# Kernel tuning notes

Measured on AMD Instinct MI355X. Metric: run time of the kernel, lower is better.

Reference implementation:

```python
import jax, jax.numpy as jnp
import numpy as np

PATCH_SIZE = [3, 5, 7]
PATCH_SEQ = [5, 7]
SEQ_SIZE = 6
WIN = 210
D_MODEL = 256
B, M = 8, 55
EPS = 1e-5


def _loo(p):
    # leave-one-out index matrix, row i = all indices except i -> (p, p-1)
    return np.array([[k for k in range(p) if k != i] for i in range(p)], dtype=np.int32)


def _mlp(x, W1, b1, W2, b2):
    # torch MLP: fc2(relu(fc1(x))), Linear weights are (out, in)
    h = jax.nn.relu(x @ W1.T + b1)
    return h @ W2.T + b2


def _forward(x, sP, nP, ssP, nsP):
    Bn, L, Mn = x.shape
    # RevIN 'norm' with fresh affine (weight=1, bias=0): identity affine; stats detached
    mean = jax.lax.stop_gradient(jnp.mean(x, axis=1, keepdims=True))
    std = jax.lax.stop_gradient(jnp.sqrt(jnp.var(x, axis=1, keepdims=True) + EPS))
    xn = (x - mean) / std
    xt = jnp.transpose(xn, (0, 2, 1)).reshape(Bn * Mn, L)  # (BM, L)
    sm, pm, ssr, psr = [], [], [], []
    for j, p in enumerate(PATCH_SIZE):
        n = L // p
        x3 = xt.reshape(Bn * Mn, p, n)  # l = r*n + k
        # size branch: leave-one-out over the p axis, blocks ordered i*n + k
        feat = jnp.transpose(x3[:, _loo(p), :], (0, 1, 3, 2)).reshape(Bn * Mn, L, p - 1)
        y = _mlp(feat, *sP[j])[..., 0]  # (BM, L)
        sm.append(jnp.transpose(y.reshape(Bn, Mn, L), (0, 2, 1)))
        # num branch: leave-one-out over the n axis of row l%p, leaving out column l//p
        g = _mlp(x3[:, :, _loo(n)], *nP[j])[..., 0]  # (BM, p, n)
        # torch cats over l (axis 0) then reshapes (B, M, L): flat order is (l, b, m)
        prior = jnp.transpose(g, (2, 1, 0)).reshape(Bn, Mn, L)  # faithful scrambled reshape
        pm.append(jnp.transpose(prior, (0, 2, 1)))
    s = SEQ_SIZE
    for j, p in enumerate(PATCH_SEQ):
        n = L // (p * s)
        x4 = xt.reshape(Bn * Mn, p, n, s)  # l = (r*n + k)*s + t
        # size_seq branch: leave-one-out over p, feature = (p-1)*s per (i, k) position
        feat = jnp.transpose(x4[:, _loo(p)], (0, 1, 3, 2, 4)).reshape(Bn * Mn, p * n, (p - 1) * s)
        y = _mlp(feat, *ssP[j])  # (BM, p*n, s)
        ssr.append(jnp.transpose(y.reshape(Bn, Mn, L), (0, 2, 1)))
        # num_seq branch: leave-one-out over n, cat order i*p + r
        featn = jnp.transpose(x4[:, :, _loo(n), :], (0, 2, 1, 3, 4)).reshape(Bn * Mn, n * p, (n - 1) * s)
        g = _mlp(featn, *nsP[j])  # (BM, n*p, s)
        d0 = PATCH_SEQ[0]  # original code hardcodes patch_seq[0] here
        h = jnp.transpose(g.reshape(Bn, Mn, (n * p) // d0, d0, s), (0, 1, 3, 2, 4)).reshape(Bn, Mn, L)
        psr.append(jnp.transpose(h, (0, 2, 1)))
    # original returns 4 lists of (B, L, M); stack all 10 for a single output
    return jnp.stack(sm + pm + ssr + psr, axis=0)


def setup_inputs() -> dict:
    key = jax.random.key(0)
    keys = iter(jax.random.split(key, 128))
    d = {"x": jax.random.normal(next(keys), (B, WIN, M), dtype=jnp.float32)}

    def lin(name, out_d, in_d):
        d[name + "W"] = jax.random.normal(next(keys), (out_d, in_d), dtype=jnp.float32) / np.float32(np.sqrt(in_d))
        d[name + "b"] = jax.random.normal(next(keys), (out_d,), dtype=jnp.float32) * np.float32(0.01)

    for j, p in enumerate(PATCH_SIZE):
        lin(f"s1_{j}", D_MODEL, p - 1)
        lin(f"s2_{j}", 1, D_MODEL)
        lin(f"n1_{j}", D_MODEL, WIN // p - 1)
        lin(f"n2_{j}", 1, D_MODEL)
    for j, p in enumerate(PATCH_SEQ):
        lin(f"ss1_{j}", D_MODEL, (p - 1) * SEQ_SIZE)
        lin(f"ss2_{j}", SEQ_SIZE, D_MODEL)
        lin(f"ns1_{j}", D_MODEL, WIN // p - SEQ_SIZE)
        lin(f"ns2_{j}", SEQ_SIZE, D_MODEL)
    return d


def reference(x, s1_0W, s1_0b, s2_0W, s2_0b, n1_0W, n1_0b, n2_0W, n2_0b,
              s1_1W, s1_1b, s2_1W, s2_1b, n1_1W, n1_1b, n2_1W, n2_1b,
              s1_2W, s1_2b, s2_2W, s2_2b, n1_2W, n1_2b, n2_2W, n2_2b,
              ss1_0W, ss1_0b, ss2_0W, ss2_0b, ns1_0W, ns1_0b, ns2_0W, ns2_0b,
              ss1_1W, ss1_1b, ss2_1W, ss2_1b, ns1_1W, ns1_1b, ns2_1W, ns2_1b):
    sP = [(s1_0W, s1_0b, s2_0W, s2_0b), (s1_1W, s1_1b, s2_1W, s2_1b), (s1_2W, s1_2b, s2_2W, s2_2b)]
    nP = [(n1_0W, n1_0b, n2_0W, n2_0b), (n1_1W, n1_1b, n2_1W, n2_1b), (n1_2W, n1_2b, n2_2W, n2_2b)]
    ssP = [(ss1_0W, ss1_0b, ss2_0W, ss2_0b), (ss1_1W, ss1_1b, ss2_1W, ss2_1b)]
    nsP = [(ns1_0W, ns1_0b, ns2_0W, ns2_0b), (ns1_1W, ns1_1b, ns2_1W, ns2_1b)]
    return _forward(x, sP, nP, ssP, nsP)
```

## Files before the change

kernel.cpp:

```cpp
#include <hip/hip_runtime.h>

#define LL  210
#define MM  55
#define NBM 440
#define DM  256
#define MLT 11550
#define BLM 92400

__device__ __forceinline__ float wave_sum(float v) {
#pragma unroll
    for (int off = 32; off > 0; off >>= 1) v += __shfl_xor(v, off, 64);
    return v;
}

__device__ __forceinline__ void fma4(float4& a, const float4 w, const float s) {
    a.x += w.x * s; a.y += w.y * s; a.z += w.z * s; a.w += w.w * s;
}
__device__ __forceinline__ void fms4(float4& a, const float4 w, const float s) {
    a.x -= w.x * s; a.y -= w.y * s; a.z -= w.z * s; a.w -= w.w * s;
}

__global__ __launch_bounds__(256) void knorm_trans(
        const float* __restrict__ x,
        const float* __restrict__ nw0, const float* __restrict__ nw1,
        const float* __restrict__ nw2,
        float* __restrict__ xt, float* __restrict__ w1t) {
    __shared__ float red[4];
    const int t = threadIdx.x;
    if (blockIdx.x < NBM) {
        const int bm = blockIdx.x, b = bm / MM, m = bm % MM;
        const int wid = t >> 6, lane = t & 63;
        float v = (t < LL) ? x[b * MLT + t * MM + m] : 0.f;
        float sv = wave_sum(v);
        if (lane == 0) red[wid] = sv;
        __syncthreads();
        float mean = (red[0] + red[1] + red[2] + red[3]) * (1.f / 210.f);
        __syncthreads();
        float dv = (t < LL) ? v - mean : 0.f;
        float sq = wave_sum(dv * dv);
        if (lane == 0) red[wid] = sq;
        __syncthreads();
        float var = (red[0] + red[1] + red[2] + red[3]) * (1.f / 210.f);
        float inv = rsqrtf(var + 1e-5f);
        if (t < LL) xt[bm * LL + t] = dv * inv;
    } else {
        int e = (int)(blockIdx.x - NBM) * 256 + t;
        const float* src; int ind, off, rel;
        if (e < 69 * DM)       { src = nw0; ind = 69; off = 0;        rel = e; }
        else if (e < 110 * DM) { src = nw1; ind = 41; off = 69 * DM;  rel = e - 69 * DM; }
        else                   { src = nw2; ind = 29; off = 110 * DM; rel = e - 110 * DM; }
        int d = rel / ind, k = rel - d * ind;
        w1t[off + k * DM + d] = src[d * ind + k];
    }
}

template <int IND>
__device__ __forceinline__ void ksize_body(const float* __restrict__ xt,
        const float* __restrict__ W1, const float* __restrict__ b1,
        const float* __restrict__ W2, const float* __restrict__ b2,
        int bm, int j, float* __restrict__ smem, float* __restrict__ out) {
    constexpr int P = IND + 1;
    constexpr int N = LL / P;
    constexpr int WPAD = (IND == 2) ? 2 : ((IND == 4) ? 4 : 8);
    float* w1p = smem;
    float* bw  = smem + DM * 8;
    float* xs  = smem + DM * 10;
    const int t = threadIdx.x;
    if (t < LL) xs[t] = xt[bm * LL + t];
    bw[2 * t]     = b1[t];
    bw[2 * t + 1] = W2[t];
    for (int e = t; e < DM * WPAD; e += 256) {
        int d = e / WPAD, c = e - d * WPAD;
        w1p[e] = (c < IND) ? W1[d * IND + c] : 0.f;
    }
    __syncthreads();
    if (t >= LL) return;
    const int l = t, i = l / N, k = l - i * N;
    float f[IND];
#pragma unroll
    for (int idx = 0; idx < IND; ++idx) {
        int row = idx < i ? idx : idx + 1;
        f[idx] = xs[row * N + k];
    }
    float y = b2[0];
#pragma unroll 4
    for (int d = 0; d < DM; ++d) {
        const float2 bwv = *(const float2*)&bw[2 * d];
        float acc = bwv.x;
        if constexpr (WPAD == 2) {
            const float2 w = *(const float2*)&w1p[d * 2];
            acc += w.x * f[0] + w.y * f[1];
        } else if constexpr (WPAD == 4) {
            const float4 w = *(const float4*)&w1p[d * 4];
            acc += w.x * f[0] + w.y * f[1] + w.z * f[2] + w.w * f[3];
        } else {
            const float4 wa = *(const float4*)&w1p[d * 8];
            const float4 wb = *(const float4*)&w1p[d * 8 + 4];
            acc += wa.x * f[0] + wa.y * f[1] + wa.z * f[2] + wa.w * f[3]
                 + wb.x * f[4] + wb.y * f[5];
        }
        y += fmaxf(acc, 0.f) * bwv.y;
    }
    const int b = bm / MM, m = bm - b * MM;
    out[j * BLM + b * MLT + l * MM + m] = y;
}

__global__ __launch_bounds__(256) void ksize_all(const float* __restrict__ xt,
        const float* __restrict__ W1_0, const float* __restrict__ b1_0, const float* __restrict__ W2_0, const float* __restrict__ b2_0,
        const float* __restrict__ W1_1, const float* __restrict__ b1_1, const float* __restrict__ W2_1, const float* __restrict__ b2_1,
        const float* __restrict__ W1_2, const float* __restrict__ b1_2, const float* __restrict__ W2_2, const float* __restrict__ b2_2,
        float* __restrict__ out) {
    __shared__ __align__(16) float smem[DM * 10 + LL];
    const int blk = blockIdx.x;
    if (blk < NBM)           ksize_body<2>(xt, W1_0, b1_0, W2_0, b2_0, blk,           0, smem, out);
    else if (blk < 2 * NBM)  ksize_body<4>(xt, W1_1, b1_1, W2_1, b2_1, blk - NBM,     1, smem, out);
    else                     ksize_body<6>(xt, W1_2, b1_2, W2_2, b2_2, blk - 2 * NBM, 2, smem, out);
}

template <int P, int N>
__device__ __forceinline__ void knum_body(const float* __restrict__ xt,
        const float* __restrict__ wt, const float* __restrict__ b1,
        const float* __restrict__ W2, const float* __restrict__ b2,
        int r, int bm0, int j, float* __restrict__ xl, float* __restrict__ out) {
    const int t = threadIdx.x;
    for (int e = t; e < 8 * N; e += 256) {
        int g = e / N, q = e - g * N;
        xl[q * 8 + g] = xt[(bm0 + g) * LL + r * N + q];
    }
    if (t < 8) xl[N * 8 + t] = 0.f;
    __syncthreads();
    const int wid = t >> 6, lane = t & 63;
    const int g0 = wid * 2;
    const float4 b1v = *(const float4*)&b1[lane * 4];
    const float4 w2v = *(const float4*)&W2[lane * 4];
    const float b2v = b2[0];
    float4 A0 = b1v, A1 = b1v;
    float4 B0 = make_float4(0.f, 0.f, 0.f, 0.f), B1 = B0;
#pragma unroll 4
    for (int q = 1; q < N; ++q) {
        const float4 w = *(const float4*)&wt[(q - 1) * DM + lane * 4];
        const float2 xv = *(const float2*)&xl[q * 8 + g0];
        fma4(B0, w, xv.x); fma4(B1, w, xv.y);
    }
    int adr[2][2];
#pragma unroll
    for (int s2 = 0; s2 < 2; ++s2) {
        int kk = lane + 64 * s2; int kc = kk < N ? kk : 0;
#pragma unroll
        for (int g = 0; g < 2; ++g) {
            int fi = (kc * P + r) * NBM + (bm0 + g0 + g);
            int ob = fi / MLT, rem = fi - ob * MLT;
            int om = rem / LL, ol = rem - om * LL;
            adr[s2][g] = (3 + j) * BLM + ob * MLT + ol * MM + om;
        }
    }
    float yA0 = 0.f, yA1 = 0.f, yB0 = 0.f, yB1 = 0.f;
#pragma unroll 2
    for (int k = 0; k < N; ++k) {
        const float4 w = *(const float4*)&wt[k * DM + lane * 4];
        const float2 xk  = *(const float2*)&xl[k * 8 + g0];
        const float2 xk1 = *(const float2*)&xl[(k + 1) * 8 + g0];
        float hx = fmaxf(A0.x + B0.x, 0.f), hy = fmaxf(A0.y + B0.y, 0.f);
        float hz = fmaxf(A0.z + B0.z, 0.f), hw = fmaxf(A0.w + B0.w, 0.f);
        float y0 = hx * w2v.x + hy * w2v.y + hz * w2v.z + hw * w2v.w;
        hx = fmaxf(A1.x + B1.x, 0.f); hy = fmaxf(A1.y + B1.y, 0.f);
        hz = fmaxf(A1.z + B1.z, 0.f); hw = fmaxf(A1.w + B1.w, 0.f);
        float y1 = hx * w2v.x + hy * w2v.y + hz * w2v.z + hw * w2v.w;
        y0 = wave_sum(y0); y1 = wave_sum(y1);
        if (k == lane)      { yA0 = y0; yA1 = y1; }
        if (k == lane + 64) { yB0 = y0; yB1 = y1; }
        fma4(A0, w, xk.x);  fma4(A1, w, xk.y);
        fms4(B0, w, xk1.x); fms4(B1, w, xk1.y);
    }
    if (lane < N)      { out[adr[0][0]] = yA0 + b2v; out[adr[0][1]] = yA1 + b2v; }
    if (lane + 64 < N) { out[adr[1][0]] = yB0 + b2v; out[adr[1][1]] = yB1 + b2v; }
}

__global__ __launch_bounds__(256) void knum_all(const float* __restrict__ xt,
        const float* __restrict__ w1t,
        const float* __restrict__ b1_0, const float* __restrict__ W2_0, const float* __restrict__ b2_0,
        const float* __restrict__ b1_1, const float* __restrict__ W2_1, const float* __restrict__ b2_1,
        const float* __restrict__ b1_2, const float* __restrict__ W2_2, const float* __restrict__ b2_2,
        float* __restrict__ out) {
    __shared__ __align__(16) float xl[71 * 8];
    const int blk = blockIdx.x;
    if (blk < 165) {
        int rel = blk;       int bm0 = (rel / 3) * 8, r = rel % 3;
        knum_body<3, 70>(xt, w1t,            b1_0, W2_0, b2_0, r, bm0, 0, xl, out);
    } else if (blk < 440) {
        int rel = blk - 165; int bm0 = (rel / 5) * 8, r = rel % 5;
        knum_body<5, 42>(xt, w1t + 69 * DM,  b1_1, W2_1, b2_1, r, bm0, 1, xl, out);
    } else {
        int rel = blk - 440; int bm0 = (rel / 7) * 8, r = rel % 7;
        knum_body<7, 30>(xt, w1t + 110 * DM, b1_2, W2_2, b2_2, r, bm0, 2, xl, out);
    }
}

template <int ISNUM, int P, int N>
__device__ __forceinline__ void kseq_body(const float* __restrict__ xt,
        const float* __restrict__ W1, const float* __restrict__ b1,
        const float* __restrict__ W2, const float* __restrict__ b2,
        int bm0, int slab, float* __restrict__ smem, float* __restrict__ out) {
    constexpr int NROWS = ISNUM ? (N - 1) : (P - 1);
    constexpr int IND = NROWS * 6;
    constexpr int WST = DM + 8;
    float* w1s  = smem;
    float* w2s  = smem + 36 * WST;
    float* b1s  = w2s + 6 * DM;
    float* b2s_ = b1s + DM;
    float* xl   = b2s_ + 8;
    const int t = threadIdx.x;
    for (int e = t; e < DM * IND; e += 256) {
        int d = e / IND, fi = e - d * IND;
        w1s[fi * WST + d] = W1[e];
    }
    for (int e = t; e < 6 * DM; e += 256) w2s[e] = W2[e];
    b1s[t] = b1[t];
    if (t < 6) b2s_[t] = b2[t];
    for (int e = t; e < 2 * LL; e += 256) {
        int g = e / LL, q = e - g * LL;
        xl[q * 2 + g] = xt[(bm0 + g) * LL + q];
    }
    __syncthreads();
    const int wid = t >> 6, lane = t & 63;
    const float4 b1v = *(const float4*)&b1s[lane * 4];
    for (int q = wid; q < 35; q += 4) {
        int a0, k0;
        if (ISNUM) { k0 = q / P; a0 = q - k0 * P; }
        else       { a0 = q / N; k0 = q - a0 * N; }
        const int pivot = ISNUM ? k0 : a0;
        float4 acc0 = b1v, acc1 = b1v;
#pragma unroll 2
        for (int idx = 0; idx < NROWS; ++idx) {
            int row = idx < pivot ? idx : idx + 1;
            int xbase = ISNUM ? (a0 * N + row) * 6 : (row * N + k0) * 6;
#pragma unroll
            for (int tt = 0; tt < 6; ++tt) {
                const float2 xv = *(const float2*)&xl[(xbase + tt) * 2];
                const float4 w = *(const float4*)&w1s[(idx * 6 + tt) * WST + lane * 4];
                fma4(acc0, w, xv.x); fma4(acc1, w, xv.y);
            }
        }
        acc0.x = fmaxf(acc0.x, 0.f); acc0.y = fmaxf(acc0.y, 0.f);
        acc0.z = fmaxf(acc0.z, 0.f); acc0.w = fmaxf(acc0.w, 0.f);
        acc1.x = fmaxf(acc1.x, 0.f); acc1.y = fmaxf(acc1.y, 0.f);
        acc1.z = fmaxf(acc1.z, 0.f); acc1.w = fmaxf(acc1.w, 0.f);
        float po0[6], po1[6];
#pragma unroll
        for (int tt = 0; tt < 6; ++tt) {
            const float4 w2v = *(const float4*)&w2s[tt * DM + lane * 4];
            float p0 = acc0.x * w2v.x + acc0.y * w2v.y + acc0.z * w2v.z + acc0.w * w2v.w;
            float p1 = acc1.x * w2v.x + acc1.y * w2v.y + acc1.z * w2v.z + acc1.w * w2v.w;
            po0[tt] = wave_sum(p0);
            po1[tt] = wave_sum(p1);
        }
        if (lane < 2) {
            const int bm = bm0 + lane;
            const int b = bm / MM, m = bm - b * MM;
            const int c2 = q / 5, dd = q - c2 * 5;
#pragma unroll
            for (int tt = 0; tt < 6; ++tt) {
                int l = ISNUM ? (dd * 42 + c2 * 6 + tt) : (q * 6 + tt);
                out[slab + b * MLT + l * MM + m] = (lane ? po1[tt] : po0[tt]) + b2s_[tt];
            }
        }
    }
}

__global__ __launch_bounds__(256) void kseq_all(const float* __restrict__ xt,
        const float* __restrict__ ss1W0, const float* __restrict__ ss1b0, const float* __restrict__ ss2W0, const float* __restrict__ ss2b0,
        const float* __restrict__ ss1W1, const float* __restrict__ ss1b1, const float* __restrict__ ss2W1, const float* __restrict__ ss2b1,
        const float* __restrict__ ns1W0, const float* __restrict__ ns1b0, const float* __restrict__ ns2W0, const float* __restrict__ ns2b0,
        const float* __restrict__ ns1W1, const float* __restrict__ ns1b1, const float* __restrict__ ns2W1, const float* __restrict__ ns2b1,
        float* __restrict__ out) {
    __shared__ __align__(16) float smem[36 * (DM + 8) + 6 * DM + DM + 8 + 2 * LL];
    const int blk = blockIdx.x;
    const int tc = blk / 220, bm0 = (blk - tc * 220) * 2;
    if (tc == 0)      kseq_body<0, 5, 7>(xt, ss1W0, ss1b0, ss2W0, ss2b0, bm0, 6 * BLM, smem, out);
    else if (tc == 1) kseq_body<0, 7, 5>(xt, ss1W1, ss1b1, ss2W1, ss2b1, bm0, 7 * BLM, smem, out);
    else if (tc == 2) kseq_body<1, 5, 7>(xt, ns1W0, ns1b0, ns2W0, ns2b0, bm0, 8 * BLM, smem, out);
    else              kseq_body<1, 7, 5>(xt, ns1W1, ns1b1, ns2W1, ns2b1, bm0, 9 * BLM, smem, out);
}

extern "C" void kernel_launch(void* const* d_in, const int* in_sizes, int n_in,
                              void* d_out, int out_size, void* d_ws, size_t ws_size,
                              hipStream_t stream) {
    (void)in_sizes; (void)n_in; (void)out_size; (void)ws_size;
    const float* x = (const float*)d_in[0];
    const float *s1W[3], *s1b[3], *s2W[3], *s2b[3], *n1W[3], *n1b[3], *n2W[3], *n2b[3];
    for (int j = 0; j < 3; ++j) {
        int base = 1 + j * 8;
        s1W[j] = (const float*)d_in[base + 0]; s1b[j] = (const float*)d_in[base + 1];
        s2W[j] = (const float*)d_in[base + 2]; s2b[j] = (const float*)d_in[base + 3];
        n1W[j] = (const float*)d_in[base + 4]; n1b[j] = (const float*)d_in[base + 5];
        n2W[j] = (const float*)d_in[base + 6]; n2b[j] = (const float*)d_in[base + 7];
    }
    const float *ss1W[2], *ss1b[2], *ss2W[2], *ss2b[2], *ns1W[2], *ns1b[2], *ns2W[2], *ns2b[2];
    for (int j = 0; j < 2; ++j) {
        int base = 25 + j * 8;
        ss1W[j] = (const float*)d_in[base + 0]; ss1b[j] = (const float*)d_in[base + 1];
        ss2W[j] = (const float*)d_in[base + 2]; ss2b[j] = (const float*)d_in[base + 3];
        ns1W[j] = (const float*)d_in[base + 4]; ns1b[j] = (const float*)d_in[base + 5];
        ns2W[j] = (const float*)d_in[base + 6]; ns2b[j] = (const float*)d_in[base + 7];
    }
    float* out = (float*)d_out;
    float* xt  = (float*)d_ws;
    float* w1t = xt + NBM * LL;

    knorm_trans<<<579, 256, 0, stream>>>(x, n1W[0], n1W[1], n1W[2], xt, w1t);
    ksize_all<<<1320, 256, 0, stream>>>(xt,
        s1W[0], s1b[0], s2W[0], s2b[0],
        s1W[1], s1b[1], s2W[1], s2b[1],
        s1W[2], s1b[2], s2W[2], s2b[2], out);
    knum_all<<<825, 256, 0, stream>>>(xt, w1t,
        n1b[0], n2W[0], n2b[0],
        n1b[1], n2W[1], n2b[1],
        n1b[2], n2W[2], n2b[2], out);
    kseq_all<<<880, 256, 0, stream>>>(xt,
        ss1W[0], ss1b[0], ss2W[0], ss2b[0],
        ss1W[1], ss1b[1], ss2W[1], ss2b[1],
        ns1W[0], ns1b[0], ns2W[0], ns2b[0],
        ns1W[1], ns1b[1], ns2W[1], ns2b[1], out);
}
```

Measured before the change: 260.6 us.

## Interleave normalized series in groups of eight and prepack all MLP weights globally

The normalization kernel now writes activations in an 8-series interleaved layout. It also pre-transposes the seq-branch first-layer weights and packs the size-branch weights into float4 records, so the consumer kernels read directly from global/L2 instead of staging through shared memory. The seq kernel processes 8 series per block with 8 accumulators, cutting the grid from 880 to 220 blocks. The num and seq kernels replace per-output wave reductions with a butterfly transpose-reduce that produces 8 results per pass. This removes shared-memory staging, syncs and redundant weight loads. In exchange it raises register pressure and gives fewer blocks in kseq, which may underfill the GPU.

```diff
diff --git a/kernel.cpp b/kernel.cpp
--- a/kernel.cpp
+++ b/kernel.cpp
@@ -7,6 +7,10 @@
 #define MLT 11550
 #define BLM 92400
 
+#define XTG_OFF  0
+#define W1T_OFF  92400
+#define REC_OFF  158704
+
 __device__ __forceinline__ float wave_sum(float v) {
 #pragma unroll
     for (int off = 32; off > 0; off >>= 1) v += __shfl_xor(v, off, 64);
@@ -20,15 +24,46 @@
     a.x -= w.x * s; a.y -= w.y * s; a.z -= w.z * s; a.w -= w.w * s;
 }
 
+__device__ __forceinline__ float bfly8(const float y[8], const int lane) {
+    float z[4];
+#pragma unroll
+    for (int i = 0; i < 4; ++i) {
+        float snd = (lane & 1) ? y[2*i] : y[2*i+1];
+        float rcv = __shfl_xor(snd, 1, 64);
+        z[i] = ((lane & 1) ? y[2*i+1] : y[2*i]) + rcv;
+    }
+    float u[2];
+#pragma unroll
+    for (int i = 0; i < 2; ++i) {
+        float snd = (lane & 2) ? z[2*i] : z[2*i+1];
+        float rcv = __shfl_xor(snd, 2, 64);
+        u[i] = ((lane & 2) ? z[2*i+1] : z[2*i]) + rcv;
+    }
+    {
+        float snd = (lane & 4) ? u[0] : u[1];
+        float rcv = __shfl_xor(snd, 4, 64);
+        float w = ((lane & 4) ? u[1] : u[0]) + rcv;
+        w += __shfl_xor(w, 8, 64);
+        w += __shfl_xor(w, 16, 64);
+        w += __shfl_xor(w, 32, 64);
+        return w;
+    }
+}
+
 __global__ __launch_bounds__(256) void knorm_trans(
         const float* __restrict__ x,
-        const float* __restrict__ nw0, const float* __restrict__ nw1,
-        const float* __restrict__ nw2,
-        float* __restrict__ xt, float* __restrict__ w1t) {
+        const float* __restrict__ nw0, const float* __restrict__ nw1, const float* __restrict__ nw2,
+        const float* __restrict__ ssw0, const float* __restrict__ ssw1,
+        const float* __restrict__ nsw0, const float* __restrict__ nsw1,
+        const float* __restrict__ s1W0, const float* __restrict__ s1b0, const float* __restrict__ s2W0,
+        const float* __restrict__ s1W1, const float* __restrict__ s1b1, const float* __restrict__ s2W1,
+        const float* __restrict__ s1W2, const float* __restrict__ s1b2, const float* __restrict__ s2W2,
+        float* __restrict__ xtg, float* __restrict__ w1t, float* __restrict__ recs) {
     __shared__ float red[4];
     const int t = threadIdx.x;
-    if (blockIdx.x < NBM) {
-        const int bm = blockIdx.x, b = bm / MM, m = bm % MM;
+    const int blk = blockIdx.x;
+    if (blk < NBM) {
+        const int bm = blk, b = bm / MM, m = bm % MM;
         const int wid = t >> 6, lane = t & 63;
         float v = (t < LL) ? x[b * MLT + t * MM + m] : 0.f;
         float sv = wave_sum(v);
@@ -42,244 +77,244 @@
         __syncthreads();
         float var = (red[0] + red[1] + red[2] + red[3]) * (1.f / 210.f);
         float inv = rsqrtf(var + 1e-5f);
-        if (t < LL) xt[bm * LL + t] = dv * inv;
+        if (t < LL) xtg[(bm >> 3) * 1680 + t * 8 + (bm & 7)] = dv * inv;
+    } else if (blk < NBM + 259) {
+        const int e = (blk - NBM) * 256 + t;
+        const int cg = e >> 8, d = e & 255;
+        const float* src; int ind, c;
+        if (cg < 69)       { src = nw0;  ind = 69; c = cg; }
+        else if (cg < 110) { src = nw1;  ind = 41; c = cg - 69; }
+        else if (cg < 139) { src = nw2;  ind = 29; c = cg - 110; }
+        else if (cg < 163) { src = ssw0; ind = 24; c = cg - 139; }
+        else if (cg < 199) { src = ssw1; ind = 36; c = cg - 163; }
+        else if (cg < 235) { src = nsw0; ind = 36; c = cg - 199; }
+        else               { src = nsw1; ind = 24; c = cg - 235; }
+        w1t[cg * DM + d] = src[d * ind + c];
     } else {
-        int e = (int)(blockIdx.x - NBM) * 256 + t;
-        const float* src; int ind, off, rel;
-        if (e < 69 * DM)       { src = nw0; ind = 69; off = 0;        rel = e; }
-        else if (e < 110 * DM) { src = nw1; ind = 41; off = 69 * DM;  rel = e - 69 * DM; }
-        else                   { src = nw2; ind = 29; off = 110 * DM; rel = e - 110 * DM; }
-        int d = rel / ind, k = rel - d * ind;
-        w1t[off + k * DM + d] = src[d * ind + k];
+        const int e = (blk - NBM - 259) * 256 + t;
+        float v;
+        if (e < 1024) {
+            int d = e >> 2, c = e & 3;
+            v = (c < 2) ? s1W0[d * 2 + c] : (c == 2 ? s1b0[d] : s2W0[d]);
+        } else if (e < 3072) {
+            int rel = e - 1024, d = rel >> 3, c = rel & 7;
+            v = (c < 4) ? s1W1[d * 4 + c] : (c == 4 ? s1b1[d] : (c == 5 ? s2W1[d] : 0.f));
+        } else {
+            int rel = e - 3072, d = rel >> 3, c = rel & 7;
+            v = (c < 6) ? s1W2[d * 6 + c] : (c == 6 ? s1b2[d] : s2W2[d]);
+        }
+        recs[e] = v;
     }
 }
 
 template <int IND>
-__device__ __forceinline__ void ksize_body(const float* __restrict__ xt,
-        const float* __restrict__ W1, const float* __restrict__ b1,
-        const float* __restrict__ W2, const float* __restrict__ b2,
-        int bm, int j, float* __restrict__ smem, float* __restrict__ out) {
-    constexpr int P = IND + 1;
-    constexpr int N = LL / P;
-    constexpr int WPAD = (IND == 2) ? 2 : ((IND == 4) ? 4 : 8);
-    float* w1p = smem;
-    float* bw  = smem + DM * 8;
-    float* xs  = smem + DM * 10;
+__device__ __forceinline__ void ksize_body(const float* __restrict__ xtg,
+        const float* __restrict__ rec, const float* __restrict__ b2,
+        int bm, int j, float* __restrict__ out) {
+    constexpr int N = LL / (IND + 1);
     const int t = threadIdx.x;
-    if (t < LL) xs[t] = xt[bm * LL + t];
-    bw[2 * t]     = b1[t];
-    bw[2 * t + 1] = W2[t];
-    for (int e = t; e < DM * WPAD; e += 256) {
-        int d = e / WPAD, c = e - d * WPAD;
-        w1p[e] = (c < IND) ? W1[d * IND + c] : 0.f;
-    }
-    __syncthreads();
     if (t >= LL) return;
-    const int l = t, i = l / N, k = l - i * N;
+    const float* xs = xtg + (bm >> 3) * 1680 + (bm & 7);
+    const int i = t / N, k = t - i * N;
     float f[IND];
 #pragma unroll
     for (int idx = 0; idx < IND; ++idx) {
-        int row = idx < i ? idx : idx + 1;
-        f[idx] = xs[row * N + k];
+        int row = idx + (idx >= i);
+        f[idx] = xs[(row * N + k) * 8];
     }
     float y = b2[0];
+    const float4* r4 = (const float4*)rec;
+    if constexpr (IND == 2) {
+#pragma unroll 8
+        for (int d = 0; d < DM; ++d) {
+            const float4 rv = r4[d];
+            y += fmaxf(rv.x * f[0] + rv.y * f[1] + rv.z, 0.f) * rv.w;
+        }
+    } else if constexpr (IND == 4) {
 #pragma unroll 4
-    for (int d = 0; d < DM; ++d) {
-        const float2 bwv = *(const float2*)&bw[2 * d];
-        float acc = bwv.x;
-        if constexpr (WPAD == 2) {
-            const float2 w = *(const float2*)&w1p[d * 2];
-            acc += w.x * f[0] + w.y * f[1];
-        } else if constexpr (WPAD == 4) {
-            const float4 w = *(const float4*)&w1p[d * 4];
-            acc += w.x * f[0] + w.y * f[1] + w.z * f[2] + w.w * f[3];
-        } else {
-            const float4 wa = *(const float4*)&w1p[d * 8];
-            const float4 wb = *(const float4*)&w1p[d * 8 + 4];
-            acc += wa.x * f[0] + wa.y * f[1] + wa.z * f[2] + wa.w * f[3]
-                 + wb.x * f[4] + wb.y * f[5];
-        }
-        y += fmaxf(acc, 0.f) * bwv.y;
-    }
-    const int b = bm / MM, m = bm - b * MM;
-    out[j * BLM + b * MLT + l * MM + m] = y;
-}
-
-__global__ __launch_bounds__(256) void ksize_all(const float* __restrict__ xt,
-        const float* __restrict__ W1_0, const float* __restrict__ b1_0, const float* __restrict__ W2_0, const float* __restrict__ b2_0,
-        const float* __restrict__ W1_1, const float* __restrict__ b1_1, const float* __restrict__ W2_1, const float* __restrict__ b2_1,
-        const float* __restrict__ W1_2, const float* __restrict__ b1_2, const float* __restrict__ W2_2, const float* __restrict__ b2_2,
+        for (int d = 0; d < DM; ++d) {
+            const float4 a = r4[2 * d], b = r4[2 * d + 1];
+            y += fmaxf(a.x*f[0] + a.y*f[1] + a.z*f[2] + a.w*f[3] + b.x, 0.f) * b.y;
+        }
+    } else {
+#pragma unroll 4
+        for (int d = 0; d < DM; ++d) {
+            const float4 a = r4[2 * d], b = r4[2 * d + 1];
+            y += fmaxf(a.x*f[0] + a.y*f[1] + a.z*f[2] + a.w*f[3] + b.x*f[4] + b.y*f[5] + b.z, 0.f) * b.w;
+        }
+    }
+    const int b_ = bm / MM, m = bm - b_ * MM;
+    out[j * BLM + b_ * MLT + t * MM + m] = y;
+}
+
+__global__ __launch_bounds__(256) void ksize_all(const float* __restrict__ xtg,
+        const float* __restrict__ recs,
+        const float* __restrict__ b2_0, const float* __restrict__ b2_1, const float* __restrict__ b2_2,
         float* __restrict__ out) {
-    __shared__ __align__(16) float smem[DM * 10 + LL];
     const int blk = blockIdx.x;
-    if (blk < NBM)           ksize_body<2>(xt, W1_0, b1_0, W2_0, b2_0, blk,           0, smem, out);
-    else if (blk < 2 * NBM)  ksize_body<4>(xt, W1_1, b1_1, W2_1, b2_1, blk - NBM,     1, smem, out);
-    else                     ksize_body<6>(xt, W1_2, b1_2, W2_2, b2_2, blk - 2 * NBM, 2, smem, out);
+    if (blk < NBM)          ksize_body<2>(xtg, recs,        b2_0, blk,           0, out);
+    else if (blk < 2 * NBM) ksize_body<4>(xtg, recs + 1024, b2_1, blk - NBM,     1, out);
+    else                    ksize_body<6>(xtg, recs + 3072, b2_2, blk - 2 * NBM, 2, out);
 }
 
 template <int P, int N>
-__device__ __forceinline__ void knum_body(const float* __restrict__ xt,
+__device__ __forceinline__ void knum_body(const float* __restrict__ xtg,
         const float* __restrict__ wt, const float* __restrict__ b1,
         const float* __restrict__ W2, const float* __restrict__ b2,
-        int r, int bm0, int j, float* __restrict__ xl, float* __restrict__ out) {
-    const int t = threadIdx.x;
-    for (int e = t; e < 8 * N; e += 256) {
-        int g = e / N, q = e - g * N;
-        xl[q * 8 + g] = xt[(bm0 + g) * LL + r * N + q];
-    }
-    if (t < 8) xl[N * 8 + t] = 0.f;
-    __syncthreads();
-    const int wid = t >> 6, lane = t & 63;
+        int grp, int r, int j, float* __restrict__ out) {
+    const int t = threadIdx.x, wid = t >> 6, lane = t & 63;
     const int g0 = wid * 2;
+    const float* xb = xtg + grp * 1680 + r * N * 8 + g0;
     const float4 b1v = *(const float4*)&b1[lane * 4];
     const float4 w2v = *(const float4*)&W2[lane * 4];
     const float b2v = b2[0];
+    const float* wl = wt + lane * 4;
     float4 A0 = b1v, A1 = b1v;
-    float4 B0 = make_float4(0.f, 0.f, 0.f, 0.f), B1 = B0;
-#pragma unroll 4
+    float4 B0 = make_float4(0.f,0.f,0.f,0.f), B1 = B0;
+#pragma unroll 2
     for (int q = 1; q < N; ++q) {
-        const float4 w = *(const float4*)&wt[(q - 1) * DM + lane * 4];
-        const float2 xv = *(const float2*)&xl[q * 8 + g0];
+        const float4 w = *(const float4*)(wl + (q - 1) * DM);
+        const float2 xv = *(const float2*)(xb + q * 8);
         fma4(B0, w, xv.x); fma4(B1, w, xv.y);
     }
-    int adr[2][2];
-#pragma unroll
-    for (int s2 = 0; s2 < 2; ++s2) {
-        int kk = lane + 64 * s2; int kc = kk < N ? kk : 0;
-#pragma unroll
-        for (int g = 0; g < 2; ++g) {
-            int fi = (kc * P + r) * NBM + (bm0 + g0 + g);
-            int ob = fi / MLT, rem = fi - ob * MLT;
-            int om = rem / LL, ol = rem - om * LL;
-            adr[s2][g] = (3 + j) * BLM + ob * MLT + ol * MM + om;
-        }
-    }
-    float yA0 = 0.f, yA1 = 0.f, yB0 = 0.f, yB1 = 0.f;
-#pragma unroll 2
-    for (int k = 0; k < N; ++k) {
-        const float4 w = *(const float4*)&wt[k * DM + lane * 4];
-        const float2 xk  = *(const float2*)&xl[k * 8 + g0];
-        const float2 xk1 = *(const float2*)&xl[(k + 1) * 8 + g0];
-        float hx = fmaxf(A0.x + B0.x, 0.f), hy = fmaxf(A0.y + B0.y, 0.f);
-        float hz = fmaxf(A0.z + B0.z, 0.f), hw = fmaxf(A0.w + B0.w, 0.f);
-        float y0 = hx * w2v.x + hy * w2v.y + hz * w2v.z + hw * w2v.w;
-        hx = fmaxf(A1.x + B1.x, 0.f); hy = fmaxf(A1.y + B1.y, 0.f);
-        hz = fmaxf(A1.z + B1.z, 0.f); hw = fmaxf(A1.w + B1.w, 0.f);
-        float y1 = hx * w2v.x + hy * w2v.y + hz * w2v.z + hw * w2v.w;
-        y0 = wave_sum(y0); y1 = wave_sum(y1);
-        if (k == lane)      { yA0 = y0; yA1 = y1; }
-        if (k == lane + 64) { yB0 = y0; yB1 = y1; }
-        fma4(A0, w, xk.x);  fma4(A1, w, xk.y);
-        fms4(B0, w, xk1.x); fms4(B1, w, xk1.y);
-    }
-    if (lane < N)      { out[adr[0][0]] = yA0 + b2v; out[adr[0][1]] = yA1 + b2v; }
-    if (lane + 64 < N) { out[adr[1][0]] = yB0 + b2v; out[adr[1][1]] = yB1 + b2v; }
-}
-
-__global__ __launch_bounds__(256) void knum_all(const float* __restrict__ xt,
+    constexpr int NFULL = N / 8, TAIL = N - NFULL * 8;
+    for (int c = 0; c <= NFULL; ++c) {
+        float y0[8], y1[8];
+        const bool full = (c < NFULL);
+#pragma unroll
+        for (int i = 0; i < 8; ++i) {
+            const int k = c * 8 + i;
+            if (full || i < TAIL) {
+                float hx = fmaxf(A0.x + B0.x, 0.f), hy = fmaxf(A0.y + B0.y, 0.f);
+                float hz = fmaxf(A0.z + B0.z, 0.f), hw = fmaxf(A0.w + B0.w, 0.f);
+                y0[i] = hx * w2v.x + hy * w2v.y + hz * w2v.z + hw * w2v.w;
+                hx = fmaxf(A1.x + B1.x, 0.f); hy = fmaxf(A1.y + B1.y, 0.f);
+                hz = fmaxf(A1.z + B1.z, 0.f); hw = fmaxf(A1.w + B1.w, 0.f);
+                y1[i] = hx * w2v.x + hy * w2v.y + hz * w2v.z + hw * w2v.w;
+                if (full || i < TAIL - 1) {
+                    const float4 w = *(const float4*)(wl + k * DM);
+                    const float2 xk  = *(const float2*)(xb + k * 8);
+                    const float2 xk1 = *(const float2*)(xb + k * 8 + 8);
+                    fma4(A0, w, xk.x);  fma4(A1, w, xk.y);
+                    fms4(B0, w, xk1.x); fms4(B1, w, xk1.y);
+                }
+            } else { y0[i] = 0.f; y1[i] = 0.f; }
+        }
+        const float v0 = bfly8(y0, lane), v1 = bfly8(y1, lane);
+        if (lane < 16) {
+            const int k = c * 8 + (lane & 7);
+            if (k < N) {
+                const int bm = grp * 8 + g0 + (lane >> 3);
+                const float val = ((lane < 8) ? v0 : v1) + b2v;
+                const int fi = (k * P + r) * NBM + bm;
+                const int ob = fi / MLT, rem = fi - ob * MLT;
+                const int om = rem / LL, ol = rem - om * LL;
+                out[(3 + j) * BLM + ob * MLT + ol * MM + om] = val;
+            }
+        }
+    }
+}
+
+__global__ __launch_bounds__(256) void knum_all(const float* __restrict__ xtg,
         const float* __restrict__ w1t,
         const float* __restrict__ b1_0, const float* __restrict__ W2_0, const float* __restrict__ b2_0,
         const float* __restrict__ b1_1, const float* __restrict__ W2_1, const float* __restrict__ b2_1,
         const float* __restrict__ b1_2, const float* __restrict__ W2_2, const float* __restrict__ b2_2,
         float* __restrict__ out) {
-    __shared__ __align__(16) float xl[71 * 8];
     const int blk = blockIdx.x;
     if (blk < 165) {
-        int rel = blk;       int bm0 = (rel / 3) * 8, r = rel % 3;
-        knum_body<3, 70>(xt, w1t,            b1_0, W2_0, b2_0, r, bm0, 0, xl, out);
+        int rel = blk;       knum_body<3, 70>(xtg, w1t,            b1_0, W2_0, b2_0, rel / 3, rel % 3, 0, out);
     } else if (blk < 440) {
-        int rel = blk - 165; int bm0 = (rel / 5) * 8, r = rel % 5;
-        knum_body<5, 42>(xt, w1t + 69 * DM,  b1_1, W2_1, b2_1, r, bm0, 1, xl, out);
+        int rel = blk - 165; knum_body<5, 42>(xtg, w1t + 69 * DM,  b1_1, W2_1, b2_1, rel / 5, rel % 5, 1, out);
     } else {
-        int rel = blk - 440; int bm0 = (rel / 7) * 8, r = rel % 7;
-        knum_body<7, 30>(xt, w1t + 110 * DM, b1_2, W2_2, b2_2, r, bm0, 2, xl, out);
+        int rel = blk - 440; knum_body<7, 30>(xtg, w1t + 110 * DM, b1_2, W2_2, b2_2, rel / 7, rel % 7, 2, out);
     }
 }
 
 template <int ISNUM, int P, int N>
-__device__ __forceinline__ void kseq_body(const float* __restrict__ xt,
-        const float* __restrict__ W1, const float* __restrict__ b1,
+__device__ __forceinline__ void kseq_body(const float* __restrict__ xtg,
+        const float* __restrict__ w1tb, const float* __restrict__ b1,
         const float* __restrict__ W2, const float* __restrict__ b2,
-        int bm0, int slab, float* __restrict__ smem, float* __restrict__ out) {
+        int grp, int slab, float* __restrict__ out) {
     constexpr int NROWS = ISNUM ? (N - 1) : (P - 1);
-    constexpr int IND = NROWS * 6;
-    constexpr int WST = DM + 8;
-    float* w1s  = smem;
-    float* w2s  = smem + 36 * WST;
-    float* b1s  = w2s + 6 * DM;
-    float* b2s_ = b1s + DM;
-    float* xl   = b2s_ + 8;
-    const int t = threadIdx.x;
-    for (int e = t; e < DM * IND; e += 256) {
-        int d = e / IND, fi = e - d * IND;
-        w1s[fi * WST + d] = W1[e];
-    }
-    for (int e = t; e < 6 * DM; e += 256) w2s[e] = W2[e];
-    b1s[t] = b1[t];
-    if (t < 6) b2s_[t] = b2[t];
-    for (int e = t; e < 2 * LL; e += 256) {
-        int g = e / LL, q = e - g * LL;
-        xl[q * 2 + g] = xt[(bm0 + g) * LL + q];
-    }
-    __syncthreads();
-    const int wid = t >> 6, lane = t & 63;
-    const float4 b1v = *(const float4*)&b1s[lane * 4];
+    const int t = threadIdx.x, wid = t >> 6, lane = t & 63;
+    const float4 b1v = *(const float4*)&b1[lane * 4];
+    const float* xg = xtg + grp * 1680;
+    float b2r[6];
+#pragma unroll
+    for (int tt = 0; tt < 6; ++tt) b2r[tt] = b2[tt];
+    const int bm = grp * 8 + (lane & 7);
+    const int b_ = bm / MM, m = bm - b_ * MM;
     for (int q = wid; q < 35; q += 4) {
-        int a0, k0;
-        if (ISNUM) { k0 = q / P; a0 = q - k0 * P; }
-        else       { a0 = q / N; k0 = q - a0 * N; }
-        const int pivot = ISNUM ? k0 : a0;
-        float4 acc0 = b1v, acc1 = b1v;
-#pragma unroll 2
+        int pivot, fix;
+        if (ISNUM) { pivot = q / P; fix = q - pivot * P; }
+        else       { pivot = q / N; fix = q - pivot * N; }
+        float4 acc[8];
+#pragma unroll
+        for (int g = 0; g < 8; ++g) acc[g] = b1v;
+        const float* wl = w1tb + lane * 4;
         for (int idx = 0; idx < NROWS; ++idx) {
-            int row = idx < pivot ? idx : idx + 1;
-            int xbase = ISNUM ? (a0 * N + row) * 6 : (row * N + k0) * 6;
+            const int row = idx + (idx >= pivot);
+            const int pos0 = ISNUM ? (fix * N + row) * 6 : (row * N + fix) * 6;
+            const float* xp = xg + pos0 * 8;
 #pragma unroll
             for (int tt = 0; tt < 6; ++tt) {
-                const float2 xv = *(const float2*)&xl[(xbase + tt) * 2];
-                const float4 w = *(const float4*)&w1s[(idx * 6 + tt) * WST + lane * 4];
-                fma4(acc0, w, xv.x); fma4(acc1, w, xv.y);
+                const float4 xa = *(const float4*)(xp + tt * 8);
+                const float4 xc = *(const float4*)(xp + tt * 8 + 4);
+                const float4 w  = *(const float4*)wl; wl += DM;
+                fma4(acc[0], w, xa.x); fma4(acc[1], w, xa.y);
+                fma4(acc[2], w, xa.z); fma4(acc[3], w, xa.w);
+                fma4(acc[4], w, xc.x); fma4(acc[5], w, xc.y);
+                fma4(acc[6], w, xc.z); fma4(acc[7], w, xc.w);
             }
         }
-        acc0.x = fmaxf(acc0.x, 0.f); acc0.y = fmaxf(acc0.y, 0.f);
-        acc0.z = fmaxf(acc0.z, 0.f); acc0.w = fmaxf(acc0.w, 0.f);
-        acc1.x = fmaxf(acc1.x, 0.f); acc1.y = fmaxf(acc1.y, 0.f);
-        acc1.z = fmaxf(acc1.z, 0.f); acc1.w = fmaxf(acc1.w, 0.f);
-        float po0[6], po1[6];
-#pragma unroll
-        for (int tt = 0; tt < 6; ++tt) {
-            const float4 w2v = *(const float4*)&w2s[tt * DM + lane * 4];
-            float p0 = acc0.x * w2v.x + acc0.y * w2v.y + acc0.z * w2v.z + acc0.w * w2v.w;
-            float p1 = acc1.x * w2v.x + acc1.y * w2v.y + acc1.z * w2v.z + acc1.w * w2v.w;
-            po0[tt] = wave_sum(p0);
-            po1[tt] = wave_sum(p1);
-        }
-        if (lane < 2) {
-            const int bm = bm0 + lane;
-            const int b = bm / MM, m = bm - b * MM;
-            const int c2 = q / 5, dd = q - c2 * 5;
-#pragma unroll
-            for (int tt = 0; tt < 6; ++tt) {
-                int l = ISNUM ? (dd * 42 + c2 * 6 + tt) : (q * 6 + tt);
-                out[slab + b * MLT + l * MM + m] = (lane ? po1[tt] : po0[tt]) + b2s_[tt];
+#pragma unroll
+        for (int g = 0; g < 8; ++g) {
+            acc[g].x = fmaxf(acc[g].x, 0.f); acc[g].y = fmaxf(acc[g].y, 0.f);
+            acc[g].z = fmaxf(acc[g].z, 0.f); acc[g].w = fmaxf(acc[g].w, 0.f);
+        }
+        const int c2 = q / 5, dd = q - c2 * 5;
+#pragma unroll
+        for (int h = 0; h < 2; ++h) {
+            float yv0[8], yv1[8], yv2[8];
+#pragma unroll
+            for (int tt2 = 0; tt2 < 3; ++tt2) {
+                const int tt = h * 3 + tt2;
+                const float4 w2v = *(const float4*)&W2[tt * DM + lane * 4];
+                float* yv = (tt2 == 0) ? yv0 : ((tt2 == 1) ? yv1 : yv2);
+#pragma unroll
+                for (int g = 0; g < 8; ++g)
+                    yv[g] = acc[g].x * w2v.x + acc[g].y * w2v.y + acc[g].z * w2v.z + acc[g].w * w2v.w;
             }
-        }
-    }
-}
-
-__global__ __launch_bounds__(256) void kseq_all(const float* __restrict__ xt,
-        const float* __restrict__ ss1W0, const float* __restrict__ ss1b0, const float* __restrict__ ss2W0, const float* __restrict__ ss2b0,
-        const float* __restrict__ ss1W1, const float* __restrict__ ss1b1, const float* __restrict__ ss2W1, const float* __restrict__ ss2b1,
-        const float* __restrict__ ns1W0, const float* __restrict__ ns1b0, const float* __restrict__ ns2W0, const float* __restrict__ ns2b0,
-        const float* __restrict__ ns1W1, const float* __restrict__ ns1b1, const float* __restrict__ ns2W1, const float* __restrict__ ns2b1,
+            const float r0 = bfly8(yv0, lane);
+            const float r1 = bfly8(yv1, lane);
+            const float r2 = bfly8(yv2, lane);
+            if (lane < 8) {
+#pragma unroll
+                for (int tt2 = 0; tt2 < 3; ++tt2) {
+                    const int tt = h * 3 + tt2;
+                    const int l = ISNUM ? (dd * 42 + c2 * 6 + tt) : (q * 6 + tt);
+                    const float rv = (tt2 == 0) ? r0 : ((tt2 == 1) ? r1 : r2);
+                    out[slab + b_ * MLT + l * MM + m] = rv + b2r[tt];
+                }
+            }
+        }
+    }
+}
+
+__global__ __launch_bounds__(256) void kseq_all(const float* __restrict__ xtg,
+        const float* __restrict__ w1t,
+        const float* __restrict__ ss1b0, const float* __restrict__ ss2W0, const float* __restrict__ ss2b0,
+        const float* __restrict__ ss1b1, const float* __restrict__ ss2W1, const float* __restrict__ ss2b1,
+        const float* __restrict__ ns1b0, const float* __restrict__ ns2W0, const float* __restrict__ ns2b0,
+        const float* __restrict__ ns1b1, const float* __restrict__ ns2W1, const float* __restrict__ ns2b1,
         float* __restrict__ out) {
-    __shared__ __align__(16) float smem[36 * (DM + 8) + 6 * DM + DM + 8 + 2 * LL];
     const int blk = blockIdx.x;
-    const int tc = blk / 220, bm0 = (blk - tc * 220) * 2;
-    if (tc == 0)      kseq_body<0, 5, 7>(xt, ss1W0, ss1b0, ss2W0, ss2b0, bm0, 6 * BLM, smem, out);
-    else if (tc == 1) kseq_body<0, 7, 5>(xt, ss1W1, ss1b1, ss2W1, ss2b1, bm0, 7 * BLM, smem, out);
-    else if (tc == 2) kseq_body<1, 5, 7>(xt, ns1W0, ns1b0, ns2W0, ns2b0, bm0, 8 * BLM, smem, out);
-    else              kseq_body<1, 7, 5>(xt, ns1W1, ns1b1, ns2W1, ns2b1, bm0, 9 * BLM, smem, out);
+    const int tc = blk / 55, grp = blk - tc * 55;
+    if (tc == 0)      kseq_body<0, 5, 7>(xtg, w1t + 139 * DM, ss1b0, ss2W0, ss2b0, grp, 6 * BLM, out);
+    else if (tc == 1) kseq_body<0, 7, 5>(xtg, w1t + 163 * DM, ss1b1, ss2W1, ss2b1, grp, 7 * BLM, out);
+    else if (tc == 2) kseq_body<1, 5, 7>(xtg, w1t + 199 * DM, ns1b0, ns2W0, ns2b0, grp, 8 * BLM, out);
+    else              kseq_body<1, 7, 5>(xtg, w1t + 235 * DM, ns1b1, ns2W1, ns2b1, grp, 9 * BLM, out);
 }
 
 extern "C" void kernel_launch(void* const* d_in, const int* in_sizes, int n_in,
@@ -303,22 +338,26 @@
         ns1W[j] = (const float*)d_in[base + 4]; ns1b[j] = (const float*)d_in[base + 5];
         ns2W[j] = (const float*)d_in[base + 6]; ns2b[j] = (const float*)d_in[base + 7];
     }
-    float* out = (float*)d_out;
-    float* xt  = (float*)d_ws;
-    float* w1t = xt + NBM * LL;
-
-    knorm_trans<<<579, 256, 0, stream>>>(x, n1W[0], n1W[1], n1W[2], xt, w1t);
-    ksize_all<<<1320, 256, 0, stream>>>(xt,
-        s1W[0], s1b[0], s2W[0], s2b[0],
-        s1W[1], s1b[1], s2W[1], s2b[1],
-        s1W[2], s1b[2], s2W[2], s2b[2], out);
-    knum_all<<<825, 256, 0, stream>>>(xt, w1t,
+    float* out  = (float*)d_out;
+    float* xtg  = (float*)d_ws + XTG_OFF;
+    float* w1t  = (float*)d_ws + W1T_OFF;
+    float* recs = (float*)d_ws + REC_OFF;
+
+    knorm_trans<<<719, 256, 0, stream>>>(x,
+        n1W[0], n1W[1], n1W[2],
+        ss1W[0], ss1W[1], ns1W[0], ns1W[1],
+        s1W[0], s1b[0], s2W[0],
+        s1W[1], s1b[1], s2W[1],
+        s1W[2], s1b[2], s2W[2],
+        xtg, w1t, recs);
+    ksize_all<<<1320, 256, 0, stream>>>(xtg, recs, s2b[0], s2b[1], s2b[2], out);
+    knum_all<<<825, 256, 0, stream>>>(xtg, w1t,
         n1b[0], n2W[0], n2b[0],
         n1b[1], n2W[1], n2b[1],
         n1b[2], n2W[2], n2b[2], out);
-    kseq_all<<<880, 256, 0, stream>>>(xt,
-        ss1W[0], ss1b[0], ss2W[0], ss2b[0],
-        ss1W[1], ss1b[1], ss2W[1], ss2b[1],
-        ns1W[0], ns1b[0], ns2W[0], ns2b[0],
-        ns1W[1], ns1b[1], ns2W[1], ns2b[1], out);
-}
+    kseq_all<<<220, 256, 0, stream>>>(xtg, w1t,
+        ss1b[0], ss2W[0], ss2b[0],
+        ss1b[1], ss2W[1], ss2b[1],
+        ns1b[0], ns2W[0], ns2b[0],
+        ns1b[1], ns2W[1], ns2b[1], out);
+}
```

After: 246.6 us. -5.4%, faster.
